# Kernel optimization log

Hardware: AMD Instinct MI355X
Metric: run time of the kernel (lower is better)

## Reference

```python
import jax, jax.numpy as jnp
import numpy as np
import math

WINDOW = 2048
EMBED = 1024
BATCH = 8


def setup_inputs() -> dict:
    key = jax.random.key(0)
    ks = jax.random.split(key, 7)
    s = 1.0 / math.sqrt(EMBED)
    return {
        "embeddings": jax.random.normal(ks[0], (BATCH, WINDOW, EMBED), dtype=jnp.float32),
        "Wq": jax.random.uniform(ks[1], (EMBED, EMBED), jnp.float32, -s, s),
        "bq": jax.random.uniform(ks[2], (EMBED,), jnp.float32, -s, s),
        "Wk": jax.random.uniform(ks[3], (EMBED, EMBED), jnp.float32, -s, s),
        "bk": jax.random.uniform(ks[4], (EMBED,), jnp.float32, -s, s),
        "Wv": jax.random.uniform(ks[5], (EMBED, EMBED), jnp.float32, -s, s),
        "bv": jax.random.uniform(ks[6], (EMBED,), jnp.float32, -s, s),
    }


def reference(embeddings, Wq, bq, Wk, bk, Wv, bv):
    # Linear layers: x @ W.T + b (torch nn.Linear convention)
    Q = jnp.einsum('bse,fe->bsf', embeddings, Wq) + bq
    K = jnp.einsum('bse,fe->bsf', embeddings, Wk) + bk
    V = jnp.einsum('bse,fe->bsf', embeddings, Wv) + bv
    scale = 1.0 / math.sqrt(EMBED)
    # [B, S, S] score matrix: A[b, i, j] = Q_i . K_j / sqrt(d)
    A = jnp.einsum('bie,bje->bij', Q, K) * scale
    # causal additive mask: -inf where j > i (strictly upper triangular)
    mask = jnp.triu(jnp.full((WINDOW, WINDOW), -jnp.inf, dtype=A.dtype), k=1)
    A = A + mask
    # NOTE: faithful to original nn.Softmax(dim=1): normalize over QUERY axis
    P = jax.nn.softmax(A, axis=1)
    return jnp.einsum('bij,bje->bie', P, V)
```

## Files before the change

kernel.cpp:

```cpp
#include <hip/hip_runtime.h>
#include <stdint.h>

#define WINDOW 2048
#define EMBED  1024
#define BATCH  8
#define MTOT   (BATCH*WINDOW)

typedef unsigned short u16;
typedef __bf16 bf16x8 __attribute__((ext_vector_type(8)));
typedef float  f32x4  __attribute__((ext_vector_type(4)));

#define BK 64
#define KSCALE 0.04508422717564447f

#define BM2 256
#define BN2 256
#define HALF2 8192
#define PLD  260
#define HALF1 4096

#define WAITVM4 asm volatile("s_waitcnt vmcnt(4)" ::: "memory")
#define WAITVM2 asm volatile("s_waitcnt vmcnt(2)" ::: "memory")
#define WAITVM0 asm volatile("s_waitcnt vmcnt(0)" ::: "memory")
#define SBAR    __builtin_amdgcn_s_barrier()

__device__ __forceinline__ u16 f2bf(float f) {
  union { float f; unsigned u; } a; a.f = f;
  unsigned r = a.u + 0x7FFF + ((a.u >> 16) & 1);
  return (u16)(r >> 16);
}
__device__ __forceinline__ float bf2f(u16 u) {
  union { unsigned u; float f; } a; a.u = ((unsigned)u) << 16;
  return a.f;
}

__device__ __forceinline__ void gload16(const u16* g, u16* l) {
  __builtin_amdgcn_global_load_lds(
      (const __attribute__((address_space(1))) unsigned int*)g,
      (__attribute__((address_space(3))) unsigned int*)l, 16, 0, 0);
}


__device__ __forceinline__ void gemm256(
    const u16* __restrict__ A, int lda,
    const u16* __restrict__ B, int ldb,
    int nt, u16* lds, f32x4 acc[8][4])
{
  const int tid  = threadIdx.x;
  const int lane = tid & 63;
  const int wid  = tid >> 6;
  const int wm   = (wid >> 2) * 128;
  const int wn   = (wid & 3) * 64;
  const int lrow = lane & 15;
  const int hi   = lane >> 4;
  u16* dA = lds;
  u16* dB = lds + 4 * HALF2;

  int aoff[8], boff[4];
  #pragma unroll
  for (int mi = 0; mi < 8; ++mi) {
    int r = wm + mi * 16 + lrow;
    aoff[mi] = r * 32 + ((hi ^ ((r >> 1) & 3)) << 3);
  }
  #pragma unroll
  for (int ni = 0; ni < 4; ++ni) {
    int r = wn + ni * 16 + lrow;
    boff[ni] = r * 32 + ((hi ^ ((r >> 1) & 3)) << 3);
  }

  const int f0 = tid, f1 = 512 + tid;
  const int r0 = f0 >> 2, r1 = f1 >> 2;
  const int c0 = (((f0 & 3) ^ ((r0 >> 1) & 3)) << 3);
  const int c1 = (((f1 & 3) ^ ((r1 >> 1) & 3)) << 3);
  const u16* pA0 = A + (size_t)r0 * lda + c0;
  const u16* pA1 = A + (size_t)r1 * lda + c1;
  const u16* pB0 = B + (size_t)r0 * ldb + c0;
  const u16* pB1 = B + (size_t)r1 * ldb + c1;
  const int d0 = f0 * 8, d1 = f1 * 8;

  gload16(pA0,      dA + d0);         gload16(pA1,      dA + d1);
  gload16(pB0,      dB + d0);         gload16(pB1,      dB + d1);
  gload16(pA0 + 32, dA + HALF2 + d0); gload16(pA1 + 32, dA + HALF2 + d1);
  gload16(pB0 + 32, dB + HALF2 + d0); gload16(pB1 + 32, dB + HALF2 + d1);
  pA0 += BK; pA1 += BK; pB0 += BK; pB1 += BK;
  WAITVM4;
  SBAR;

  for (int t = 0; t < nt; ++t) {
    const int cb = (t & 1) * 2;
    const int nb = ((t + 1) & 1) * 2;
    u16* LA0 = dA + cb * HALF2;  u16* LA1 = LA0 + HALF2;
    u16* LB0 = dB + cb * HALF2;  u16* LB1 = LB0 + HALF2;
    const bool s = (t + 1) < nt;
    bf16x8 av[8], bv[4];

    #pragma unroll
    for (int mi = 0; mi < 8; ++mi) av[mi] = *(const bf16x8*)(LA0 + aoff[mi]);
    #pragma unroll
    for (int ni = 0; ni < 4; ++ni) bv[ni] = *(const bf16x8*)(LB0 + boff[ni]);
    if (s) {
      gload16(pA0, dA + nb * HALF2 + d0); gload16(pA1, dA + nb * HALF2 + d1);
      gload16(pB0, dB + nb * HALF2 + d0); gload16(pB1, dB + nb * HALF2 + d1);
    }
    __builtin_amdgcn_s_setprio(1);
    #pragma unroll
    for (int mi = 0; mi < 8; ++mi)
      #pragma unroll
      for (int ni = 0; ni < 4; ++ni)
        acc[mi][ni] = __builtin_amdgcn_mfma_f32_16x16x32_bf16(av[mi], bv[ni], acc[mi][ni], 0, 0, 0);
    __builtin_amdgcn_s_setprio(0);
    if (s) { WAITVM4; } else { WAITVM0; }
    SBAR;

    #pragma unroll
    for (int mi = 0; mi < 8; ++mi) av[mi] = *(const bf16x8*)(LA1 + aoff[mi]);
    #pragma unroll
    for (int ni = 0; ni < 4; ++ni) bv[ni] = *(const bf16x8*)(LB1 + boff[ni]);
    if (s) {
      gload16(pA0 + 32, dA + nb * HALF2 + HALF2 + d0); gload16(pA1 + 32, dA + nb * HALF2 + HALF2 + d1);
      gload16(pB0 + 32, dB + nb * HALF2 + HALF2 + d0); gload16(pB1 + 32, dB + nb * HALF2 + HALF2 + d1);
      pA0 += BK; pA1 += BK; pB0 += BK; pB1 += BK;
    }
    __builtin_amdgcn_s_setprio(1);
    #pragma unroll
    for (int mi = 0; mi < 8; ++mi)
      #pragma unroll
      for (int ni = 0; ni < 4; ++ni)
        acc[mi][ni] = __builtin_amdgcn_mfma_f32_16x16x32_bf16(av[mi], bv[ni], acc[mi][ni], 0, 0, 0);
    __builtin_amdgcn_s_setprio(0);
    if (s) { WAITVM4; }
    SBAR;
  }
}

__device__ __forceinline__ void gemm128(
    const u16* __restrict__ A, int lda,
    const u16* __restrict__ B, int ldb,
    int nt, u16* lds, f32x4 acc[4][2])
{
  const int tid  = threadIdx.x;
  const int lane = tid & 63;
  const int wid  = tid >> 6;
  const int wm   = (wid >> 2) * 64;
  const int wn   = (wid & 3) * 32;
  const int lrow = lane & 15;
  const int hi   = lane >> 4;
  u16* dA = lds;
  u16* dB = lds + 4 * HALF1;

  const int r = tid >> 2;
  const int cs = (((tid & 3) ^ ((r >> 1) & 3)) << 3);
  const u16* pA = A + (size_t)r * lda + cs;
  const u16* pB = B + (size_t)r * ldb + cs;
  const int d = tid * 8;

  gload16(pA,      dA + d);         gload16(pB,      dB + d);
  gload16(pA + 32, dA + HALF1 + d); gload16(pB + 32, dB + HALF1 + d);
  pA += BK; pB += BK;
  WAITVM2;
  SBAR;

  for (int t = 0; t < nt; ++t) {
    const int cur = (t & 1) * 2;
    const int nxt = ((t + 1) & 1) * 2;
    u16* LA0 = dA + cur * HALF1;  u16* LA1 = LA0 + HALF1;
    u16* LB0 = dB + cur * HALF1;  u16* LB1 = LB0 + HALF1;
    const bool s = (t + 1) < nt;
    bf16x8 av[4], bv[2];

    #pragma unroll
    for (int mi = 0; mi < 4; ++mi) {
      int rr = wm + mi * 16 + lrow;
      av[mi] = *(const bf16x8*)(LA0 + rr * 32 + ((hi ^ ((rr >> 1) & 3)) << 3));
    }
    #pragma unroll
    for (int ni = 0; ni < 2; ++ni) {
      int rr = wn + ni * 16 + lrow;
      bv[ni] = *(const bf16x8*)(LB0 + rr * 32 + ((hi ^ ((rr >> 1) & 3)) << 3));
    }
    if (s) { gload16(pA, dA + nxt * HALF1 + d); gload16(pB, dB + nxt * HALF1 + d); }
    #pragma unroll
    for (int mi = 0; mi < 4; ++mi)
      #pragma unroll
      for (int ni = 0; ni < 2; ++ni)
        acc[mi][ni] = __builtin_amdgcn_mfma_f32_16x16x32_bf16(av[mi], bv[ni], acc[mi][ni], 0, 0, 0);
    if (s) { WAITVM2; } else { WAITVM0; }
    SBAR;

    #pragma unroll
    for (int mi = 0; mi < 4; ++mi) {
      int rr = wm + mi * 16 + lrow;
      av[mi] = *(const bf16x8*)(LA1 + rr * 32 + ((hi ^ ((rr >> 1) & 3)) << 3));
    }
    #pragma unroll
    for (int ni = 0; ni < 2; ++ni) {
      int rr = wn + ni * 16 + lrow;
      bv[ni] = *(const bf16x8*)(LB1 + rr * 32 + ((hi ^ ((rr >> 1) & 3)) << 3));
    }
    if (s) {
      gload16(pA + 32, dA + nxt * HALF1 + HALF1 + d);
      gload16(pB + 32, dB + nxt * HALF1 + HALF1 + d);
      pA += BK; pB += BK;
    }
    #pragma unroll
    for (int mi = 0; mi < 4; ++mi)
      #pragma unroll
      for (int ni = 0; ni < 2; ++ni)
        acc[mi][ni] = __builtin_amdgcn_mfma_f32_16x16x32_bf16(av[mi], bv[ni], acc[mi][ni], 0, 0, 0);
    if (s) { WAITVM2; }
    SBAR;
  }
}

__global__ __launch_bounds__(256) void k_w(const float* __restrict__ Wq,
                                           const float* __restrict__ bk,
                                           float* __restrict__ w) {
  const int e  = blockIdx.x * 256 + threadIdx.x;
  const int f0 = blockIdx.y * 64;
  float acc = 0.f;
  #pragma unroll 8
  for (int f = 0; f < 64; ++f)
    acc += Wq[(size_t)(f0 + f) * EMBED + e] * bk[f0 + f];
  atomicAdd(&w[e], acc * KSCALE);
}

__global__ __launch_bounds__(256) void k_cvtu(const float* __restrict__ X,
                                              const float* __restrict__ w,
                                              u16* __restrict__ Xb,
                                              float* __restrict__ u) {
  const int row = blockIdx.x;
  const int tid = threadIdx.x;
  float4 v  = *(const float4*)(X + (size_t)row * EMBED + tid * 4);
  float4 ww = *(const float4*)(w + tid * 4);
  ushort4 o;
  o.x = f2bf(v.x); o.y = f2bf(v.y); o.z = f2bf(v.z); o.w = f2bf(v.w);
  *(ushort4*)(Xb + (size_t)row * EMBED + tid * 4) = o;
  float p = v.x * ww.x + v.y * ww.y + v.z * ww.z + v.w * ww.w;
  #pragma unroll
  for (int off = 1; off < 64; off <<= 1) p += __shfl_xor(p, off, 64);
  __shared__ float red[4];
  if ((tid & 63) == 0) red[tid >> 6] = p;
  __syncthreads();
  if (tid == 0) u[row] = red[0] + red[1] + red[2] + red[3];
}

__global__ __launch_bounds__(256) void k_trw(const float* __restrict__ Wq,
                                             const float* __restrict__ Wk,
                                             u16* __restrict__ WqT,
                                             u16* __restrict__ WkT) {
  __shared__ u16 tile[64][68];
  const float* in = blockIdx.z ? Wk : Wq;
  u16* out        = blockIdx.z ? WkT : WqT;
  const int f0 = blockIdx.x * 64, e0 = blockIdx.y * 64;
  const int t = threadIdx.x;
  const int rr = t >> 4;
  const int cc = (t & 15) * 4;
  #pragma unroll
  for (int p = 0; p < 4; ++p) {
    int r = p * 16 + rr;
    float4 v = *(const float4*)(in + (size_t)(f0 + r) * EMBED + e0 + cc);
    tile[r][cc + 0] = f2bf(v.x); tile[r][cc + 1] = f2bf(v.y);
    tile[r][cc + 2] = f2bf(v.z); tile[r][cc + 3] = f2bf(v.w);
  }
  __syncthreads();
  #pragma unroll
  for (int p = 0; p < 4; ++p) {
    int er = p * 16 + rr;
    ushort4 o;
    o.x = tile[cc + 0][er]; o.y = tile[cc + 1][er];
    o.z = tile[cc + 2][er]; o.w = tile[cc + 3][er];
    *(ushort4*)(out + (size_t)(e0 + er) * EMBED + f0 + cc) = o;
  }
}

__global__ __launch_bounds__(256) void k_cvt(const float* __restrict__ in,
                                             u16* __restrict__ out, int n) {
  int i = (blockIdx.x * 256 + threadIdx.x) * 4;
  if (i >= n) return;
  float4 v = *(const float4*)(in + i);
  ushort4 o;
  o.x = f2bf(v.x); o.y = f2bf(v.y); o.z = f2bf(v.z); o.w = f2bf(v.w);
  *(ushort4*)(out + i) = o;
}

__global__ __launch_bounds__(512, 4) void k_H(const u16* __restrict__ WkT,
                                              const u16* __restrict__ WqT,
                                              float* __restrict__ Hws) {
  __shared__ u16 lds[8 * HALF1];
  const int s  = blockIdx.x & 3;
  const int tt = blockIdx.x >> 2;
  const int a0 = (tt >> 3) * 128, b0 = (tt & 7) * 128;
  const u16* A = WkT + (size_t)a0 * EMBED + s * 256;
  const u16* B = WqT + (size_t)b0 * EMBED + s * 256;
  f32x4 acc[4][2];
  const f32x4 zz = {0.f,0.f,0.f,0.f};
  #pragma unroll
  for (int i = 0; i < 4; ++i) for (int j = 0; j < 2; ++j) acc[i][j] = zz;
  gemm128(A, EMBED, B, EMBED, 4, lds, acc);

  float* Hp = Hws + (size_t)s * EMBED * EMBED;
  const int lane = threadIdx.x & 63, wid = threadIdx.x >> 6;
  const int wm = (wid >> 2) * 64, wn = (wid & 3) * 32;
  const int lrow = lane & 15, hi = lane >> 4;
  #pragma unroll
  for (int mi = 0; mi < 4; ++mi)
    #pragma unroll
    for (int ni = 0; ni < 2; ++ni)
      #pragma unroll
      for (int rr = 0; rr < 4; ++rr) {
        int ga = a0 + wm + mi * 16 + hi * 4 + rr;
        int gb = b0 + wn + ni * 16 + lrow;
        Hp[(size_t)ga * EMBED + gb] = acc[mi][ni][rr];
      }
}

__global__ __launch_bounds__(256) void k_Hred(const float* __restrict__ Hws,
                                              u16* __restrict__ H) {
  const size_t N = (size_t)EMBED * EMBED;
  int i = (blockIdx.x * 256 + threadIdx.x) * 4;
  float4 a = *(const float4*)(Hws + i);
  float4 b = *(const float4*)(Hws + N + i);
  float4 c = *(const float4*)(Hws + 2 * N + i);
  float4 d = *(const float4*)(Hws + 3 * N + i);
  ushort4 o;
  o.x = f2bf((a.x + b.x + c.x + d.x) * KSCALE);
  o.y = f2bf((a.y + b.y + c.y + d.y) * KSCALE);
  o.z = f2bf((a.z + b.z + c.z + d.z) * KSCALE);
  o.w = f2bf((a.w + b.w + c.w + d.w) * KSCALE);
  *(ushort4*)(H + i) = o;
}

__global__ __launch_bounds__(512, 2) void k_yv(
    const u16* __restrict__ Xb, const u16* __restrict__ H,
    const u16* __restrict__ Wvb, const float* __restrict__ bv,
    u16* __restrict__ Yb, u16* __restrict__ Vb)
{
  __shared__ u16 lds[8 * HALF2];
  const int m0 = blockIdx.x * BM2;
  const int n0 = blockIdx.y * BN2;
  const int z  = blockIdx.z;
  const u16* Bop = z ? Wvb : H;
  u16* out       = z ? Vb : Yb;

  f32x4 acc[8][4];
  const f32x4 zz = {0.f,0.f,0.f,0.f};
  #pragma unroll
  for (int i = 0; i < 8; ++i) for (int j = 0; j < 4; ++j) acc[i][j] = zz;
  gemm256(Xb + (size_t)m0 * EMBED, EMBED, Bop + (size_t)n0 * EMBED, EMBED,
          EMBED / BK, lds, acc);

  const int lane = threadIdx.x & 63, wid = threadIdx.x >> 6;
  const int wm = (wid >> 2) * 128, wn = (wid & 3) * 64;
  const int lrow = lane & 15, hi = lane >> 4;
  #pragma unroll
  for (int mi = 0; mi < 8; ++mi)
    #pragma unroll
    for (int ni = 0; ni < 4; ++ni)
      #pragma unroll
      for (int rr = 0; rr < 4; ++rr) {
        int gm = m0 + wm + mi * 16 + hi * 4 + rr;
        int gn = n0 + wn + ni * 16 + lrow;
        float bb = z ? bv[gn] : 0.0f;
        out[(size_t)gm * EMBED + gn] = f2bf(acc[mi][ni][rr] + bb);
      }
}

__global__ __launch_bounds__(512, 2) void k_spd(
    const u16* __restrict__ Y, const u16* __restrict__ Xb,
    const float* __restrict__ u, u16* __restrict__ P, float* __restrict__ D)
{
  const int s   = blockIdx.x;
  const int xcd = s & 7;
  const int q   = s >> 3;
  int it = 0;
  while (q >= ((it + 1) * (it + 2)) / 2) ++it;
  const int jt = q - (it * (it + 1)) / 2;
  const int b  = (xcd - it) & 7;
  const int i0 = it * BM2;
  const int j0 = jt * BN2;

  __shared__ u16 lds[BM2 * PLD];
  const u16* A = Y  + (size_t)b * WINDOW * EMBED + (size_t)i0 * EMBED;
  const u16* B = Xb + (size_t)b * WINDOW * EMBED + (size_t)j0 * EMBED;
  f32x4 acc[8][4];
  const f32x4 zz = {0.f,0.f,0.f,0.f};
  #pragma unroll
  for (int i = 0; i < 8; ++i) for (int j = 0; j < 4; ++j) acc[i][j] = zz;
  gemm256(A, EMBED, B, EMBED, EMBED / BK, lds, acc);

  u16* Pb   = P + (size_t)b * WINDOW * WINDOW;
  float* Db = D + (size_t)b * WINDOW;
  const float* ub = u + (size_t)b * WINDOW;
  const int tid  = threadIdx.x;
  const int lane = tid & 63, wid = tid >> 6;
  const int wm = (wid >> 2) * 128, wn = (wid & 3) * 64;
  const int lrow = lane & 15, hi = lane >> 4;

  #pragma unroll
  for (int ni = 0; ni < 4; ++ni) {
    int lj = wn + ni * 16 + lrow;
    float csum = 0.f;
    #pragma unroll
    for (int mi = 0; mi < 8; ++mi)
      #pragma unroll
      for (int rr = 0; rr < 4; ++rr) {
        int li = wm + mi * 16 + hi * 4 + rr;
        float p = ((i0 + li) >= (j0 + lj))
                    ? exp2f(acc[mi][ni][rr] + ub[i0 + li]) : 0.0f;
        lds[li * PLD + lj] = f2bf(p);
        csum += p;
      }
    csum += __shfl_xor(csum, 16, 64);
    csum += __shfl_xor(csum, 32, 64);
    if (hi == 0) atomicAdd(&Db[j0 + lj], csum);
  }
  __syncthreads();

  #pragma unroll
  for (int it2 = 0; it2 < 16; ++it2) {
    int f   = it2 * 512 + tid;
    int row = f >> 5;
    int c   = f & 31;
    bf16x8 v = *(const bf16x8*)(lds + row * PLD + c * 8);
    *(bf16x8*)(Pb + (size_t)(i0 + row) * WINDOW + j0 + c * 8) = v;
  }
}

__global__ __launch_bounds__(256) void k_vdt(
    const u16* __restrict__ V, const float* __restrict__ D, u16* __restrict__ Vdt)
{
  __shared__ u16 tile[64][68];
  const int j0 = blockIdx.x * 64, e0 = blockIdx.y * 64, b = blockIdx.z;
  const u16* Vb = V   + (size_t)b * WINDOW * EMBED;
  u16* Tb       = Vdt + (size_t)b * EMBED * WINDOW;
  const float* Db = D + (size_t)b * WINDOW;
  const int t = threadIdx.x;
  const int rr = t >> 4;
  const int cc = (t & 15) * 4;
  #pragma unroll
  for (int p = 0; p < 4; ++p) {
    int r = p * 16 + rr;
    *(uint2*)&tile[r][cc] = *(const uint2*)(Vb + (size_t)(j0 + r) * EMBED + e0 + cc);
  }
  __syncthreads();
  #pragma unroll
  for (int p = 0; p < 4; ++p) {
    int er = p * 16 + rr;
    ushort4 o;
    o.x = f2bf(bf2f(tile[cc + 0][er]) / Db[j0 + cc + 0]);
    o.y = f2bf(bf2f(tile[cc + 1][er]) / Db[j0 + cc + 1]);
    o.z = f2bf(bf2f(tile[cc + 2][er]) / Db[j0 + cc + 2]);
    o.w = f2bf(bf2f(tile[cc + 3][er]) / Db[j0 + cc + 3]);
    *(ushort4*)(Tb + (size_t)(e0 + er) * WINDOW + j0 + cc) = o;
  }
}

__global__ __launch_bounds__(512, 2) void k_out(
    const u16* __restrict__ P, const u16* __restrict__ Vdt, float* __restrict__ O)
{
  __shared__ u16 lds[8 * HALF2];
  const int s   = blockIdx.x;
  const int xcd = s & 7;
  const int q   = s >> 3;
  const int et  = q & 3;
  const int it  = 7 - (q >> 2);
  const int b   = (xcd - it) & 7;
  const int i0  = it * BM2;
  const int e0  = et * BN2;

  const u16* A = P   + (size_t)b * WINDOW * WINDOW + (size_t)i0 * WINDOW;
  const u16* B = Vdt + (size_t)b * EMBED * WINDOW  + (size_t)e0 * WINDOW;
  f32x4 acc[8][4];
  const f32x4 zz = {0.f,0.f,0.f,0.f};
  #pragma unroll
  for (int i = 0; i < 8; ++i) for (int j = 0; j < 4; ++j) acc[i][j] = zz;
  gemm256(A, WINDOW, B, WINDOW, (i0 + BM2) / BK, lds, acc);

  float* Ob = O + (size_t)b * WINDOW * EMBED;
  const int lane = threadIdx.x & 63, wid = threadIdx.x >> 6;
  const int wm = (wid >> 2) * 128, wn = (wid & 3) * 64;
  const int lrow = lane & 15, hi = lane >> 4;
  #pragma unroll
  for (int mi = 0; mi < 8; ++mi)
    #pragma unroll
    for (int ni = 0; ni < 4; ++ni)
      #pragma unroll
      for (int rr = 0; rr < 4; ++rr) {
        int gi = i0 + wm + mi * 16 + hi * 4 + rr;
        int ge = e0 + wn + ni * 16 + lrow;
        Ob[(size_t)gi * EMBED + ge] = acc[mi][ni][rr];
      }
}

extern "C" void kernel_launch(void* const* d_in, const int* in_sizes, int n_in,
                              void* d_out, int out_size, void* d_ws, size_t ws_size,
                              hipStream_t stream) {
  const float* X  = (const float*)d_in[0];
  const float* Wq = (const float*)d_in[1];
  const float* bq = (const float*)d_in[2];
  const float* Wk = (const float*)d_in[3];
  const float* bk = (const float*)d_in[4];
  const float* Wv = (const float*)d_in[5];
  const float* bv = (const float*)d_in[6];
  float* O = (float*)d_out;
  (void)bq;

  char* ws = (char*)d_ws;
  size_t off = 0;
  auto alloc = [&](size_t bytes) -> void* {
    void* p = ws + off; off += (bytes + 255) & ~(size_t)255; return p;
  };
  u16*   Xb  = (u16*)alloc((size_t)MTOT * EMBED * 2);
  u16*   Yb  = (u16*)alloc((size_t)MTOT * EMBED * 2);
  u16*   Vb  = (u16*)alloc((size_t)MTOT * EMBED * 2);
  u16*   Vdt = (u16*)alloc((size_t)BATCH * EMBED * WINDOW * 2);
  u16*   P   = (u16*)alloc((size_t)BATCH * WINDOW * WINDOW * 2);
  u16*   WqT = (u16*)alloc((size_t)EMBED * EMBED * 2);
  u16*   WkT = (u16*)alloc((size_t)EMBED * EMBED * 2);
  u16*   Wvb = (u16*)alloc((size_t)EMBED * EMBED * 2);
  u16*   H   = (u16*)alloc((size_t)EMBED * EMBED * 2);
  float* Hws = (float*)alloc((size_t)4 * EMBED * EMBED * 4);
  float* w   = (float*)alloc((size_t)EMBED * 4);
  float* u   = (float*)alloc((size_t)MTOT * 4);
  float* D   = (float*)alloc((size_t)MTOT * 4);
  (void)ws_size; (void)in_sizes; (void)n_in; (void)out_size;

  (void)hipMemsetAsync(w, 0, (size_t)EMBED * 4, stream);
  k_w<<<dim3(EMBED / 256, 16), 256, 0, stream>>>(Wq, bk, w);
  k_cvtu<<<dim3(MTOT), 256, 0, stream>>>(X, w, Xb, u);
  k_trw<<<dim3(16, 16, 2), 256, 0, stream>>>(Wq, Wk, WqT, WkT);
  k_cvt<<<dim3(EMBED * EMBED / 1024), 256, 0, stream>>>(Wv, Wvb, EMBED * EMBED);
  k_H<<<dim3(256), 512, 0, stream>>>(WkT, WqT, Hws);
  k_Hred<<<dim3(EMBED * EMBED / 1024), 256, 0, stream>>>(Hws, H);

  k_yv<<<dim3(MTOT / BM2, EMBED / BN2, 2), 512, 0, stream>>>(Xb, H, Wvb, bv, Yb, Vb);

  (void)hipMemsetAsync(D, 0, (size_t)MTOT * 4, stream);
  k_spd<<<dim3(288), 512, 0, stream>>>(Yb, Xb, u, P, D);

  k_vdt<<<dim3(WINDOW / 64, EMBED / 64, BATCH), 256, 0, stream>>>(Vb, D, Vdt);

  k_out<<<dim3(256), 512, 0, stream>>>(P, Vdt, O);
}
```

Before: 307.5 us.

## Fuse Wv conversion into transpose kernel and drop split-K reduction for H

Result: faster. 285.1 us (-7.3%).

```diff
diff --git a/kernel.cpp b/kernel.cpp
--- a/kernel.cpp
+++ b/kernel.cpp
@@ -246,15 +246,30 @@
 
 __global__ __launch_bounds__(256) void k_trw(const float* __restrict__ Wq,
                                              const float* __restrict__ Wk,
+                                             const float* __restrict__ Wv,
                                              u16* __restrict__ WqT,
-                                             u16* __restrict__ WkT) {
+                                             u16* __restrict__ WkT,
+                                             u16* __restrict__ Wvb) {
   __shared__ u16 tile[64][68];
-  const float* in = blockIdx.z ? Wk : Wq;
-  u16* out        = blockIdx.z ? WkT : WqT;
+  const int z  = blockIdx.z;
   const int f0 = blockIdx.x * 64, e0 = blockIdx.y * 64;
-  const int t = threadIdx.x;
+  const int t  = threadIdx.x;
   const int rr = t >> 4;
   const int cc = (t & 15) * 4;
+
+  if (z == 2) {
+    #pragma unroll
+    for (int p = 0; p < 4; ++p) {
+      int r = p * 16 + rr;
+      float4 v = *(const float4*)(Wv + (size_t)(f0 + r) * EMBED + e0 + cc);
+      ushort4 o;
+      o.x = f2bf(v.x); o.y = f2bf(v.y); o.z = f2bf(v.z); o.w = f2bf(v.w);
+      *(ushort4*)(Wvb + (size_t)(f0 + r) * EMBED + e0 + cc) = o;
+    }
+    return;
+  }
+  const float* in = z ? Wk : Wq;
+  u16* out        = z ? WkT : WqT;
   #pragma unroll
   for (int p = 0; p < 4; ++p) {
     int r = p * 16 + rr;
@@ -273,32 +288,19 @@
   }
 }
 
-__global__ __launch_bounds__(256) void k_cvt(const float* __restrict__ in,
-                                             u16* __restrict__ out, int n) {
-  int i = (blockIdx.x * 256 + threadIdx.x) * 4;
-  if (i >= n) return;
-  float4 v = *(const float4*)(in + i);
-  ushort4 o;
-  o.x = f2bf(v.x); o.y = f2bf(v.y); o.z = f2bf(v.z); o.w = f2bf(v.w);
-  *(ushort4*)(out + i) = o;
-}
-
 __global__ __launch_bounds__(512, 4) void k_H(const u16* __restrict__ WkT,
                                               const u16* __restrict__ WqT,
-                                              float* __restrict__ Hws) {
+                                              u16* __restrict__ H) {
   __shared__ u16 lds[8 * HALF1];
-  const int s  = blockIdx.x & 3;
-  const int tt = blockIdx.x >> 2;
+  const int tt = blockIdx.x;
   const int a0 = (tt >> 3) * 128, b0 = (tt & 7) * 128;
-  const u16* A = WkT + (size_t)a0 * EMBED + s * 256;
-  const u16* B = WqT + (size_t)b0 * EMBED + s * 256;
   f32x4 acc[4][2];
   const f32x4 zz = {0.f,0.f,0.f,0.f};
   #pragma unroll
   for (int i = 0; i < 4; ++i) for (int j = 0; j < 2; ++j) acc[i][j] = zz;
-  gemm128(A, EMBED, B, EMBED, 4, lds, acc);
-
-  float* Hp = Hws + (size_t)s * EMBED * EMBED;
+  gemm128(WkT + (size_t)a0 * EMBED, EMBED, WqT + (size_t)b0 * EMBED, EMBED,
+          EMBED / BK, lds, acc);
+
   const int lane = threadIdx.x & 63, wid = threadIdx.x >> 6;
   const int wm = (wid >> 2) * 64, wn = (wid & 3) * 32;
   const int lrow = lane & 15, hi = lane >> 4;
@@ -310,24 +312,8 @@
       for (int rr = 0; rr < 4; ++rr) {
         int ga = a0 + wm + mi * 16 + hi * 4 + rr;
         int gb = b0 + wn + ni * 16 + lrow;
-        Hp[(size_t)ga * EMBED + gb] = acc[mi][ni][rr];
+        H[(size_t)ga * EMBED + gb] = f2bf(acc[mi][ni][rr] * KSCALE);
       }
-}
-
-__global__ __launch_bounds__(256) void k_Hred(const float* __restrict__ Hws,
-                                              u16* __restrict__ H) {
-  const size_t N = (size_t)EMBED * EMBED;
-  int i = (blockIdx.x * 256 + threadIdx.x) * 4;
-  float4 a = *(const float4*)(Hws + i);
-  float4 b = *(const float4*)(Hws + N + i);
-  float4 c = *(const float4*)(Hws + 2 * N + i);
-  float4 d = *(const float4*)(Hws + 3 * N + i);
-  ushort4 o;
-  o.x = f2bf((a.x + b.x + c.x + d.x) * KSCALE);
-  o.y = f2bf((a.y + b.y + c.y + d.y) * KSCALE);
-  o.z = f2bf((a.z + b.z + c.z + d.z) * KSCALE);
-  o.w = f2bf((a.w + b.w + c.w + d.w) * KSCALE);
-  *(ushort4*)(H + i) = o;
 }
 
 __global__ __launch_bounds__(512, 2) void k_yv(
@@ -396,6 +382,13 @@
   const int wm = (wid >> 2) * 128, wn = (wid & 3) * 64;
   const int lrow = lane & 15, hi = lane >> 4;
 
+  float uu[8][4];
+  #pragma unroll
+  for (int mi = 0; mi < 8; ++mi)
+    #pragma unroll
+    for (int rr = 0; rr < 4; ++rr)
+      uu[mi][rr] = ub[i0 + wm + mi * 16 + hi * 4 + rr];
+
   #pragma unroll
   for (int ni = 0; ni < 4; ++ni) {
     int lj = wn + ni * 16 + lrow;
@@ -406,7 +399,7 @@
       for (int rr = 0; rr < 4; ++rr) {
         int li = wm + mi * 16 + hi * 4 + rr;
         float p = ((i0 + li) >= (j0 + lj))
-                    ? exp2f(acc[mi][ni][rr] + ub[i0 + li]) : 0.0f;
+                    ? exp2f(acc[mi][ni][rr] + uu[mi][rr]) : 0.0f;
         lds[li * PLD + lj] = f2bf(p);
         csum += p;
       }
@@ -519,7 +512,6 @@
   u16*   WkT = (u16*)alloc((size_t)EMBED * EMBED * 2);
   u16*   Wvb = (u16*)alloc((size_t)EMBED * EMBED * 2);
   u16*   H   = (u16*)alloc((size_t)EMBED * EMBED * 2);
-  float* Hws = (float*)alloc((size_t)4 * EMBED * EMBED * 4);
   float* w   = (float*)alloc((size_t)EMBED * 4);
   float* u   = (float*)alloc((size_t)MTOT * 4);
   float* D   = (float*)alloc((size_t)MTOT * 4);
@@ -528,10 +520,8 @@
   (void)hipMemsetAsync(w, 0, (size_t)EMBED * 4, stream);
   k_w<<<dim3(EMBED / 256, 16), 256, 0, stream>>>(Wq, bk, w);
   k_cvtu<<<dim3(MTOT), 256, 0, stream>>>(X, w, Xb, u);
-  k_trw<<<dim3(16, 16, 2), 256, 0, stream>>>(Wq, Wk, WqT, WkT);
-  k_cvt<<<dim3(EMBED * EMBED / 1024), 256, 0, stream>>>(Wv, Wvb, EMBED * EMBED);
-  k_H<<<dim3(256), 512, 0, stream>>>(WkT, WqT, Hws);
-  k_Hred<<<dim3(EMBED * EMBED / 1024), 256, 0, stream>>>(Hws, H);
+  k_trw<<<dim3(16, 16, 3), 256, 0, stream>>>(Wq, Wk, Wv, WqT, WkT, Wvb);
+  k_H<<<dim3(64), 512, 0, stream>>>(WkT, WqT, H);
 
   k_yv<<<dim3(MTOT / BM2, EMBED / BN2, 2), 512, 0, stream>>>(Xb, H, Wvb, bv, Yb, Vb);
 
```
